# Performance work log

Measured on AMD Instinct MI355X. Metric: run time of the kernel, lower is better.

Reference implementation:

```python
import jax, jax.numpy as jnp
import numpy as np

MAX_LEN, BATCH, EMB = 512, 32, 41
HID, UNITS = 800, 20
BOND_LENS = jnp.array([1.329, 1.459, 1.525], jnp.float32)
BOND_ANGLES = jnp.array([2.034, 2.119, 1.937], jnp.float32)
INIT_ABC = jnp.array([[0.0, 0.0, 1.0], [0.0, 1.0, 0.0], [1.0, 0.0, 0.0]], jnp.float32)


def _lstm_dir(x, w_ih, w_hh, b, reverse):
    # x: [T, B, in]; returns hidden states [T, B, H]
    T, B, _ = x.shape
    H = w_hh.shape[1]
    xs = jnp.flip(x, 0) if reverse else x
    xw = jnp.einsum('tbi,gi->tbg', xs, w_ih) + b  # precompute input projection

    def step(carry, xt):
        h, c = carry
        gates = xt + h @ w_hh.T
        i, f, g, o = jnp.split(gates, 4, axis=-1)
        c = jax.nn.sigmoid(f) * c + jax.nn.sigmoid(i) * jnp.tanh(g)
        h = jax.nn.sigmoid(o) * jnp.tanh(c)
        return (h, c), h

    init = (jnp.zeros((B, H), x.dtype), jnp.zeros((B, H), x.dtype))
    _, hs = jax.lax.scan(step, init, xw)
    return jnp.flip(hs, 0) if reverse else hs


def _bilstm_layer(x, w_ih, w_hh, b):
    # w_ih: [2, 4H, in]; w_hh: [2, 4H, H]; b: [2, 4H]
    fwd = _lstm_dir(x, w_ih[0], w_hh[0], b[0], False)
    bwd = _lstm_dir(x, w_ih[1], w_hh[1], b[1], True)
    return jnp.concatenate([fwd, bwd], axis=-1)


def _geometric_unit(coords3, triplet):
    # coords3: [3, B, 3] last three atoms; triplet: [B, 3] torsion angles
    A, Bc, C = coords3[0], coords3[1], coords3[2]
    new = []
    for i in range(3):
        Tang, R, P = BOND_ANGLES[i], BOND_LENS[i], triplet[:, i]
        D2 = jnp.stack([-R * jnp.cos(Tang) * jnp.ones_like(P),
                        R * jnp.cos(P) * jnp.sin(Tang),
                        R * jnp.sin(P) * jnp.sin(Tang)], axis=1)  # [B,3]
        BC = C - Bc
        bc = BC / jnp.linalg.norm(BC, axis=1, keepdims=True)
        AB = Bc - A
        N = jnp.cross(AB, bc)
        n = N / jnp.linalg.norm(N, axis=1, keepdims=True)
        M = jnp.stack([bc, jnp.cross(n, bc), n], axis=2)  # [B,3,3]
        D = jnp.einsum('bij,bj->bi', M, D2) + C
        A, Bc, C = Bc, C, D
        new.append(D)
    return jnp.stack([A, Bc, C]), jnp.stack(new)  # carry, [3,B,3]


def setup_inputs() -> dict:
    key = jax.random.key(0)
    ks = jax.random.split(key, 10)
    k = 1.0 / np.sqrt(HID)
    u = lambda kk, shp, lim: jax.random.uniform(kk, shp, jnp.float32, -lim, lim)
    in0, in1 = EMB + 1, 2 * HID
    return {
        'sequences': jax.random.normal(ks[0], (MAX_LEN, BATCH, EMB), jnp.float32),
        'lengths': jnp.full((BATCH,), MAX_LEN, jnp.int64 if jax.config.jax_enable_x64 else jnp.int32),
        'w_ih0': u(ks[1], (2, 4 * HID, in0), k),
        'w_hh0': u(ks[2], (2, 4 * HID, HID), k),
        'b0': u(ks[3], (2, 4 * HID), k),
        'w_ih1': u(ks[4], (2, 4 * HID, in1), k),
        'w_hh1': u(ks[5], (2, 4 * HID, HID), k),
        'b1': u(ks[6], (2, 4 * HID), k),
        'lin_w': u(ks[7], (UNITS, 2 * HID), 1.0 / np.sqrt(2 * HID)),
        'lin_b': u(ks[8], (UNITS,), 1.0 / np.sqrt(2 * HID)),
        'alphabet': jax.random.uniform(ks[9], (UNITS, 3), jnp.float32, -3.14, 3.14),
    }


def reference(sequences, lengths, w_ih0, w_hh0, b0, w_ih1, w_hh1, b1, lin_w, lin_b, alphabet):
    T, B, _ = sequences.shape
    abs_pos = jnp.broadcast_to(jnp.arange(T, dtype=sequences.dtype)[:, None, None], (T, B, 1))
    x = jnp.concatenate([sequences, abs_pos], axis=2)  # [T, B, EMB+1]
    # 2-layer bidirectional LSTM (all lengths == max_len -> packing is identity)
    h = _bilstm_layer(x, w_ih0, w_hh0, b0)
    h = _bilstm_layer(h, w_ih1, w_hh1, b1)  # [T, B, 2H]
    # linear -> softmax over alphabet, trig angle decode
    soft = jax.nn.softmax(h @ lin_w.T + lin_b, axis=2)  # [T, B, UNITS]
    sine = soft @ jnp.sin(alphabet)   # [T, B, 3]
    cosine = soft @ jnp.cos(alphabet)
    out = jnp.arctan2(sine, cosine)   # torsion angle triplets
    # sequential geometric coordinate recurrence over timesteps 1..T-1
    init = jnp.broadcast_to(INIT_ABC[:, None, :], (3, B, 3))
    _, new_coords = jax.lax.scan(_geometric_unit, init, out[1:])  # [T-1, 3, B, 3]
    pred_coords = jnp.concatenate([init, new_coords.reshape(-1, B, 3)], axis=0)
    return pred_coords  # [3 + 3*(T-1), B, 3]
```

## Files before the change

### kernel.cpp

```cpp
#include <hip/hip_runtime.h>
#include <math.h>

#define T_LEN 512
#define NB    32
#define EMB_  41
#define IN0_  42
#define HID_  800
#define G4_   3200
#define IN1_  1600
#define NU    20
#define NCH   100

typedef unsigned short u16;
typedef unsigned int   u32;
typedef unsigned long long u64;
typedef __attribute__((ext_vector_type(8))) short short8;
typedef __attribute__((ext_vector_type(4))) float f32x4;

__device__ __forceinline__ float bf2f(u16 v) {
    union { u32 u; float f; } c; c.u = ((u32)v) << 16; return c.f;
}
__device__ __forceinline__ u16 f2bf(float f) {
    union { float f; u32 u; } c; c.f = f;
    u32 r = (c.u + 0x7fffu + ((c.u >> 16) & 1u)) >> 16;
    return (u16)r;
}
__device__ __forceinline__ short cvt_hl(float v, int hl) {
    u16 hi = f2bf(v);
    return hl ? (short)f2bf(v - bf2f(hi)) : (short)hi;
}
__device__ __forceinline__ f32x4 mfma16(short8 a, short8 b, f32x4 c) {
    return __builtin_amdgcn_mfma_f32_16x16x32_bf16(a, b, c, 0, 0, 0);
}
__device__ __forceinline__ u64 aload(const u64* p) {
    return __hip_atomic_load(p, __ATOMIC_RELAXED, __HIP_MEMORY_SCOPE_AGENT);
}
__device__ __forceinline__ void astore(u64* p, u64 v) {
    __hip_atomic_store(p, v, __ATOMIC_RELAXED, __HIP_MEMORY_SCOPE_AGENT);
}
__device__ __forceinline__ int afload(const int* p) {
    return __hip_atomic_load(p, __ATOMIC_RELAXED, __HIP_MEMORY_SCOPE_AGENT);
}
__device__ __forceinline__ void afstore(int* p, int v) {
    __hip_atomic_store(p, v, __ATOMIC_RELAXED, __HIP_MEMORY_SCOPE_AGENT);
}

__global__ __launch_bounds__(256, 1)
void lstm0_persist(const float* __restrict__ seq, const float* __restrict__ wih0,
                   const float* __restrict__ whh0, const float* __restrict__ bias,
                   u16* __restrict__ h0f, u16* __restrict__ hB, int* __restrict__ flags)
{
    __shared__ __align__(16) float part[2048];
    __shared__ __align__(16) u16 stageB[25600];
    __shared__ __align__(16) float w0l[32*48];
    __shared__ __align__(16) float xsl[32*48];
    __shared__ u16 hpk[NB*8];
    const int tid = threadIdx.x;
    const int d = blockIdx.x / NCH, ch = blockIdx.x % NCH;
    const int w = tid >> 6, l = tid & 63;
    const int p = w & 1, hl = w >> 1;
    int* myflags = flags + d*NCH*16;

    short8 wreg[25];
    {
        const int m = l & 15, g = p*2 + (m>>3), j = ch*8 + (m&7);
        const float* base = whh0 + ((size_t)(d*G4_ + g*HID_ + j))*HID_ + (l>>4)*8;
#pragma unroll
        for (int kc = 0; kc < 25; ++kc) {
            float4 f0 = *(const float4*)(base + kc*32);
            float4 f1 = *(const float4*)(base + kc*32 + 4);
            short8 v;
            v[0]=cvt_hl(f0.x,hl); v[1]=cvt_hl(f0.y,hl); v[2]=cvt_hl(f0.z,hl); v[3]=cvt_hl(f0.w,hl);
            v[4]=cvt_hl(f1.x,hl); v[5]=cvt_hl(f1.y,hl); v[6]=cvt_hl(f1.z,hl); v[7]=cvt_hl(f1.w,hl);
            wreg[kc] = v;
        }
    }
    for (int idx = tid; idx < 32*EMB_; idx += 256) {
        int r = idx / EMB_, k = idx % EMB_;
        int ju_ = r >> 2, g = r & 3;
        w0l[r*48 + k] = wih0[((size_t)(d*G4_ + g*HID_ + ch*8 + ju_))*IN0_ + k];
    }
    const int ju = tid >> 5, b = tid & 31;
    const int j = ch*8 + ju;
    const int nt = b >> 4, n = b & 15;
    float biasr[4], wpos[4];
#pragma unroll
    for (int g = 0; g < 4; ++g) {
        biasr[g] = bias[d*G4_ + g*HID_ + j];
        wpos[g]  = wih0[((size_t)(d*G4_ + g*HID_ + j))*IN0_ + EMB_];
    }
    float creg = 0.f;
    __syncthreads();

    for (int s = 0; s < T_LEN; ++s) {
        const int t = d ? (T_LEN-1-s) : s;
        const u64* hq64 = (const u64*)(hB + (size_t)((s&1)*2 + d)*25600);
        u64*      hnq  = (u64*)(hB + (size_t)(((s&1)^1)*2 + d)*25600);

        for (int idx = tid; idx < 32*EMB_; idx += 256)
            xsl[(idx/EMB_)*48 + idx%EMB_] = seq[(size_t)t*(NB*EMB_) + idx];

        if (s > 0 && tid < NCH)
            while (afload(myflags + tid*16) < s) __builtin_amdgcn_s_sleep(1);
        __syncthreads();

        {
            u64 tmp[25];
#pragma unroll
            for (int q = 0; q < 25; ++q) tmp[q] = aload(hq64 + tid + q*256);
#pragma unroll
            for (int q = 0; q < 25; ++q) ((u64*)stageB)[tid + q*256] = tmp[q];
        }
        __syncthreads();

        f32x4 acc0 = {0.f,0.f,0.f,0.f}, acc1 = {0.f,0.f,0.f,0.f};
#pragma unroll 5
        for (int kc = 0; kc < 25; ++kc) {
            short8 b0 = *(const short8*)(stageB + kc*1024 + l*8);
            short8 b1 = *(const short8*)(stageB + kc*1024 + 512 + l*8);
            acc0 = mfma16(wreg[kc], b0, acc0);
            acc1 = mfma16(wreg[kc], b1, acc1);
        }
        {
            const int mrow = (l>>4)*4, nn = l & 15;
#pragma unroll
            for (int r = 0; r < 4; ++r) {
                part[(((p*2+hl)*2 + 0)*16 + mrow + r)*16 + nn] = acc0[r];
                part[(((p*2+hl)*2 + 1)*16 + mrow + r)*16 + nn] = acc1[r];
            }
        }
        __syncthreads();

        float dot0 = 0.f, dot1 = 0.f, dot2 = 0.f, dot3 = 0.f;
        {
            const float* wr = &w0l[ju*4*48];
            const float* xr = &xsl[b*48];
#pragma unroll
            for (int k4 = 0; k4 < 40; k4 += 4) {
                float4 xk = *(const float4*)(xr + k4);
                float4 w0 = *(const float4*)(wr + 0*48 + k4);
                float4 w1 = *(const float4*)(wr + 1*48 + k4);
                float4 w2 = *(const float4*)(wr + 2*48 + k4);
                float4 w3 = *(const float4*)(wr + 3*48 + k4);
                dot0 += w0.x*xk.x + w0.y*xk.y + w0.z*xk.z + w0.w*xk.w;
                dot1 += w1.x*xk.x + w1.y*xk.y + w1.z*xk.z + w1.w*xk.w;
                dot2 += w2.x*xk.x + w2.y*xk.y + w2.z*xk.z + w2.w*xk.w;
                dot3 += w3.x*xk.x + w3.y*xk.y + w3.z*xk.z + w3.w*xk.w;
            }
            float xk = xr[40];
            dot0 += wr[0*48+40]*xk; dot1 += wr[1*48+40]*xk;
            dot2 += wr[2*48+40]*xk; dot3 += wr[3*48+40]*xk;
        }
        float v[4] = {dot0, dot1, dot2, dot3};
#pragma unroll
        for (int g = 0; g < 4; ++g) {
            const int pp = g >> 1, m = (g & 1)*8 + ju;
            v[g] += part[(((pp*2+0)*2 + nt)*16 + m)*16 + n]
                  + part[(((pp*2+1)*2 + nt)*16 + m)*16 + n]
                  + biasr[g] + (float)t * wpos[g];
        }
        float ig = 1.f/(1.f + expf(-v[0]));
        float fg = 1.f/(1.f + expf(-v[1]));
        float gg = tanhf(v[2]);
        float og = 1.f/(1.f + expf(-v[3]));
        creg = fg * creg + ig * gg;
        hpk[b*8 + ju] = f2bf(og * tanhf(creg));
        __syncthreads();

        u64 pk = 0; int xoff = 0;
        if (tid < 64) {
            const int bb = tid >> 1, half = tid & 1;
            const u16* hp = &hpk[bb*8 + half*4];
            pk = (u64)hp[0] | ((u64)hp[1]<<16) | ((u64)hp[2]<<32) | ((u64)hp[3]<<48);
            const int ntb = bb >> 4, llb = ((ch&3)<<4) | (bb&15);
            astore(hnq + ((ch>>2)*2 + ntb)*128 + llb*2 + half, pk);
            xoff = ((d*25 + (ch>>2))*2 + ntb)*128 + llb*2 + half;
        }
        __syncthreads();
        if (tid == 0) afstore(myflags + ch*16, s+1);
        if (tid < 64)
            ((u64*)(h0f + (size_t)t*51200))[xoff] = pk;
    }
}

__global__ __launch_bounds__(256, 1)
void lstm1_persist(const float* __restrict__ wih1, const float* __restrict__ whh1,
                   const float* __restrict__ bias, const float* __restrict__ lin_w,
                   const u16* __restrict__ h0f, u16* __restrict__ hB,
                   int* __restrict__ flags, float* __restrict__ logits)
{
    __shared__ __align__(16) u16 wihL[2*50*512];
    __shared__ __align__(16) u16 stageB[25600];
    __shared__ __align__(16) float part[2048];
    __shared__ u16 hpk[NB*8];
    const int tid = threadIdx.x;
    const int d = blockIdx.x / NCH, ch = blockIdx.x % NCH;
    const int w = tid >> 6, l = tid & 63;
    const int p = w & 1, hl = w >> 1;
    int* myflags = flags + d*NCH*16;

    short8 wreg[25];
    {
        const int m = l & 15, g = p*2 + (m>>3), j = ch*8 + (m&7);
        const float* base = whh1 + ((size_t)(d*G4_ + g*HID_ + j))*HID_ + (l>>4)*8;
#pragma unroll
        for (int kc = 0; kc < 25; ++kc) {
            float4 f0 = *(const float4*)(base + kc*32);
            float4 f1 = *(const float4*)(base + kc*32 + 4);
            short8 v;
            v[0]=cvt_hl(f0.x,hl); v[1]=cvt_hl(f0.y,hl); v[2]=cvt_hl(f0.z,hl); v[3]=cvt_hl(f0.w,hl);
            v[4]=cvt_hl(f1.x,hl); v[5]=cvt_hl(f1.y,hl); v[6]=cvt_hl(f1.z,hl); v[7]=cvt_hl(f1.w,hl);
            wreg[kc] = v;
        }
    }
    for (int o = tid; o < 6400; o += 256) {
        int pp = o / 3200, r = o % 3200, kc = r >> 6, ll = r & 63;
        int m = ll & 15, g = pp*2 + (m>>3), jj = ch*8 + (m&7);
        const float* base = wih1 + ((size_t)(d*G4_ + g*HID_ + jj))*IN1_ + kc*32 + (ll>>4)*8;
        float4 f0 = *(const float4*)base;
        float4 f1 = *(const float4*)(base + 4);
        short8 v;
        v[0]=(short)f2bf(f0.x); v[1]=(short)f2bf(f0.y); v[2]=(short)f2bf(f0.z); v[3]=(short)f2bf(f0.w);
        v[4]=(short)f2bf(f1.x); v[5]=(short)f2bf(f1.y); v[6]=(short)f2bf(f1.z); v[7]=(short)f2bf(f1.w);
        *(short8*)&wihL[o*8] = v;
    }
    const int ol = tid >> 5, ln = tid & 31;
    const int lo = ch*7 + ol;
    const bool lown = (ol < 7) && (lo < NB*NU);
    int lofs = 0;
    float wlin[25];
    if (lown) {
        const int bb = lo / NU, uu = lo % NU;
        lofs = (bb >> 4)*512 + ((((ln >> 3) << 4) | (bb & 15)))*8 + (ln & 7);
        const float* wrow = lin_w + (size_t)uu*IN1_ + d*HID_ + ln;
#pragma unroll
        for (int i = 0; i < 25; ++i) wlin[i] = wrow[i*32];
    }
    const int ju = tid >> 5, b = tid & 31;
    const int j = ch*8 + ju;
    const int nt = b >> 4, n = b & 15;
    float biasr[4];
#pragma unroll
    for (int g = 0; g < 4; ++g) biasr[g] = bias[d*G4_ + g*HID_ + j];
    float creg = 0.f;
    __syncthreads();

    for (int s = 0; s < T_LEN; ++s) {
        const int t = d ? (T_LEN-1-s) : s;
        const u64* hq64 = (const u64*)(hB + (size_t)((s&1)*2 + d)*25600);
        u64*      hnq  = (u64*)(hB + (size_t)(((s&1)^1)*2 + d)*25600);

        f32x4 acc0 = {0.f,0.f,0.f,0.f}, acc1 = {0.f,0.f,0.f,0.f};
        {
            const u16* xb = h0f + (size_t)t*51200;
#pragma unroll 5
            for (int kc = 0; kc < 25; ++kc) {
                const int idx = hl*25 + kc;
                short8 a  = *(const short8*)&wihL[(p*50 + idx)*512 + l*8];
                short8 b0 = *(const short8*)(xb + idx*1024 + l*8);
                short8 b1 = *(const short8*)(xb + idx*1024 + 512 + l*8);
                acc0 = mfma16(a, b0, acc0);
                acc1 = mfma16(a, b1, acc1);
            }
        }

        if (s > 0 && tid < NCH)
            while (afload(myflags + tid*16) < s) __builtin_amdgcn_s_sleep(1);
        __syncthreads();

        {
            u64 tmp[25];
#pragma unroll
            for (int q = 0; q < 25; ++q) tmp[q] = aload(hq64 + tid + q*256);
#pragma unroll
            for (int q = 0; q < 25; ++q) ((u64*)stageB)[tid + q*256] = tmp[q];
        }
        __syncthreads();

#pragma unroll 5
        for (int kc = 0; kc < 25; ++kc) {
            short8 b0 = *(const short8*)(stageB + kc*1024 + l*8);
            short8 b1 = *(const short8*)(stageB + kc*1024 + 512 + l*8);
            acc0 = mfma16(wreg[kc], b0, acc0);
            acc1 = mfma16(wreg[kc], b1, acc1);
        }
        {
            const int mrow = (l>>4)*4, nn = l & 15;
#pragma unroll
            for (int r = 0; r < 4; ++r) {
                part[(((p*2+hl)*2 + 0)*16 + mrow + r)*16 + nn] = acc0[r];
                part[(((p*2+hl)*2 + 1)*16 + mrow + r)*16 + nn] = acc1[r];
            }
        }
        __syncthreads();

        float v[4];
#pragma unroll
        for (int g = 0; g < 4; ++g) {
            const int pp = g >> 1, m = (g & 1)*8 + ju;
            v[g] = part[(((pp*2+0)*2 + nt)*16 + m)*16 + n]
                 + part[(((pp*2+1)*2 + nt)*16 + m)*16 + n] + biasr[g];
        }
        float ig = 1.f/(1.f + expf(-v[0]));
        float fg = 1.f/(1.f + expf(-v[1]));
        float gg = tanhf(v[2]);
        float og = 1.f/(1.f + expf(-v[3]));
        creg = fg * creg + ig * gg;
        float hn = og * tanhf(creg);
        hpk[b*8 + ju] = f2bf(hn);
        __syncthreads();

        if (tid < 64) {
            const int bb = tid >> 1, half = tid & 1;
            const u16* hp = &hpk[bb*8 + half*4];
            u64 pk = (u64)hp[0] | ((u64)hp[1]<<16) | ((u64)hp[2]<<32) | ((u64)hp[3]<<48);
            const int ntb = bb >> 4, llb = ((ch&3)<<4) | (bb&15);
            astore(hnq + ((ch>>2)*2 + ntb)*128 + llb*2 + half, pk);
        }
        __syncthreads();
        if (tid == 0) afstore(myflags + ch*16, s+1);

        if (s > 0 && lown) {
            float sum = 0.f;
#pragma unroll
            for (int i = 0; i < 25; ++i)
                sum += bf2f(stageB[i*1024 + lofs]) * wlin[i];
#pragma unroll
            for (int off2 = 16; off2; off2 >>= 1) sum += __shfl_down(sum, off2, 32);
            if (ln == 0) {
                const int tprev = d ? (T_LEN - s) : (s - 1);
                logits[((size_t)d*T_LEN + tprev)*640 + lo] = sum;
            }
        }
    }
    if (tid < NCH)
        while (afload(myflags + tid*16) < T_LEN) __builtin_amdgcn_s_sleep(1);
    __syncthreads();
    {
        const u64* hq64 = (const u64*)(hB + (size_t)((T_LEN&1)*2 + d)*25600);
        u64 tmp[25];
#pragma unroll
        for (int q = 0; q < 25; ++q) tmp[q] = aload(hq64 + tid + q*256);
#pragma unroll
        for (int q = 0; q < 25; ++q) ((u64*)stageB)[tid + q*256] = tmp[q];
    }
    __syncthreads();
    if (lown) {
        float sum = 0.f;
#pragma unroll
        for (int i = 0; i < 25; ++i)
            sum += bf2f(stageB[i*1024 + lofs]) * wlin[i];
#pragma unroll
        for (int off2 = 16; off2; off2 >>= 1) sum += __shfl_down(sum, off2, 32);
        if (ln == 0) {
            const int tprev = d ? 0 : (T_LEN - 1);
            logits[((size_t)d*T_LEN + tprev)*640 + lo] = sum;
        }
    }
}

__global__ __launch_bounds__(256)
void epilogue(const float* __restrict__ logits, const float* __restrict__ lin_b,
              const float* __restrict__ alphabet, float* __restrict__ cs)
{
    __shared__ float sa[NU*3], ca[NU*3], lb[NU];
    const int tid = threadIdx.x;
    if (tid < NU*3) { float al = alphabet[tid]; sa[tid] = sinf(al); ca[tid] = cosf(al); }
    if (tid < NU) lb[tid] = lin_b[tid];
    __syncthreads();
    const int row = blockIdx.x*256 + tid;
    if (row >= T_LEN*NB) return;
    const int t = row >> 5, b = row & 31;
    float lg[NU];
    float m = -1e30f;
#pragma unroll 4
    for (int u = 0; u < NU; ++u) {
        lg[u] = lb[u] + logits[(size_t)t*640 + b*NU + u]
                      + logits[((size_t)T_LEN + t)*640 + b*NU + u];
        m = fmaxf(m, lg[u]);
    }
    float ssum = 0.f;
#pragma unroll 4
    for (int u = 0; u < NU; ++u) { lg[u] = expf(lg[u] - m); ssum += lg[u]; }
    float inv = 1.f / ssum;
#pragma unroll
    for (int i = 0; i < 3; ++i) {
        float sv = 0.f, cv = 0.f;
#pragma unroll 4
        for (int u = 0; u < NU; ++u) {
            float sw = lg[u] * inv;
            sv += sw * sa[u*3 + i];
            cv += sw * ca[u*3 + i];
        }
        float rinv = rsqrtf(fmaxf(sv*sv + cv*cv, 1e-30f));
        *(float2*)(cs + ((size_t)row*3 + i)*2) = make_float2(cv*rinv, sv*rinv);
    }
}

__global__ __launch_bounds__(64)
void geometry(const float* __restrict__ cs, float* __restrict__ out)
{
    const int b = threadIdx.x;
    if (b >= NB) return;
    const float blen[3] = {1.329f, 1.459f, 1.525f};
    const float bang[3] = {2.034f, 2.119f, 1.937f};
    float sT[3], cT[3];
#pragma unroll
    for (int i = 0; i < 3; ++i) { sT[i] = sinf(bang[i]); cT[i] = cosf(bang[i]); }

    float Ax=0.f,Ay=0.f,Az=1.f, Bx=0.f,By=1.f,Bz=0.f, Cx=1.f,Cy=0.f,Cz=0.f;
    out[(0*NB + b)*3 + 0] = 0.f; out[(0*NB + b)*3 + 1] = 0.f; out[(0*NB + b)*3 + 2] = 1.f;
    out[(1*NB + b)*3 + 0] = 0.f; out[(1*NB + b)*3 + 1] = 1.f; out[(1*NB + b)*3 + 2] = 0.f;
    out[(2*NB + b)*3 + 0] = 1.f; out[(2*NB + b)*3 + 1] = 0.f; out[(2*NB + b)*3 + 2] = 0.f;

    for (int t = 1; t < T_LEN; ++t) {
        float2 pc[3];
#pragma unroll
        for (int i = 0; i < 3; ++i)
            pc[i] = *(const float2*)(cs + (((size_t)t*NB + b)*3 + i)*2);
#pragma unroll
        for (int i = 0; i < 3; ++i) {
            float R = blen[i];
            float d2x = -R*cT[i], d2y = R*pc[i].x*sT[i], d2z = R*pc[i].y*sT[i];
            float bcx = Cx-Bx, bcy = Cy-By, bcz = Cz-Bz;
            float inv = rsqrtf(bcx*bcx + bcy*bcy + bcz*bcz);
            bcx *= inv; bcy *= inv; bcz *= inv;
            float abx = Bx-Ax, aby = By-Ay, abz = Bz-Az;
            float nx = aby*bcz - abz*bcy;
            float ny = abz*bcx - abx*bcz;
            float nz = abx*bcy - aby*bcx;
            inv = rsqrtf(fmaxf(nx*nx + ny*ny + nz*nz, 1e-30f));
            nx *= inv; ny *= inv; nz *= inv;
            float mx = ny*bcz - nz*bcy;
            float my = nz*bcx - nx*bcz;
            float mz = nx*bcy - ny*bcx;
            float Dx = bcx*d2x + mx*d2y + nx*d2z + Cx;
            float Dy = bcy*d2x + my*d2y + ny*d2z + Cy;
            float Dz = bcz*d2x + mz*d2y + nz*d2z + Cz;
            Ax=Bx; Ay=By; Az=Bz; Bx=Cx; By=Cy; Bz=Cz; Cx=Dx; Cy=Dy; Cz=Dz;
            const int r = 3 + (t-1)*3 + i;
            out[((size_t)r*NB + b)*3 + 0] = Dx;
            out[((size_t)r*NB + b)*3 + 1] = Dy;
            out[((size_t)r*NB + b)*3 + 2] = Dz;
        }
    }
}

extern "C" void kernel_launch(void* const* d_in, const int* in_sizes, int n_in,
                              void* d_out, int out_size, void* d_ws, size_t ws_size,
                              hipStream_t stream)
{
    (void)in_sizes; (void)n_in; (void)out_size; (void)ws_size;
    const float* seq   = (const float*)d_in[0];
    const float* w_ih0 = (const float*)d_in[2];
    const float* w_hh0 = (const float*)d_in[3];
    const float* b0    = (const float*)d_in[4];
    const float* w_ih1 = (const float*)d_in[5];
    const float* w_hh1 = (const float*)d_in[6];
    const float* b1    = (const float*)d_in[7];
    const float* lin_w = (const float*)d_in[8];
    const float* lin_b = (const float*)d_in[9];
    const float* alpha = (const float*)d_in[10];

    char* ws = (char*)d_ws;
    size_t off = 0;
    u16* h0f   = (u16*)(ws + off); off += 52428800ull;
    u16* hB    = (u16*)(ws + off); off += 204800ull;
    int* flagsL0 = (int*)(ws + off); off += 12800ull;
    int* flagsL1 = (int*)(ws + off); off += 12800ull;
    float* logits = (float*)(ws + off); off += 2621440ull;
    float* cs = (float*)(ws + off); off += 393216ull;

    hipMemsetAsync(hB, 0, 204800 + 12800 + 12800, stream);

    lstm0_persist<<<dim3(2*NCH), dim3(256), 0, stream>>>(seq, w_ih0, w_hh0, b0, h0f, hB, flagsL0);

    hipMemsetAsync(hB, 0, 204800, stream);
    lstm1_persist<<<dim3(2*NCH), dim3(256), 0, stream>>>(w_ih1, w_hh1, b1, lin_w, h0f, hB,
                                                         flagsL1, logits);

    epilogue<<<dim3(64), dim3(256), 0, stream>>>(logits, lin_b, alpha, cs);
    geometry<<<dim3(1), dim3(64), 0, stream>>>(cs, (float*)d_out);
}
```

Before: 9.470 ms.

## Read recurrent state from full history buffers and pack progress flags densely

Each layer's persistent kernel drops the double-buffered hB exchange buffer. It now reads the previous step's hidden state straight from the per-timestep output history (h0f, or a new h1f for layer 1) using plain loads instead of atomic loads. Step 0 zero-fills the staging buffer. Progress flags are packed contiguously instead of padded to 64 bytes, which removes the separate state stores and a memset but may add false sharing on the flag line. Plain loads of data written by other blocks rely on the flag acquire ordering and cache coherence at agent scope, which the relaxed atomics may not guarantee.

```diff
diff --git a/kernel.cpp b/kernel.cpp
--- a/kernel.cpp
+++ b/kernel.cpp
@@ -32,9 +32,6 @@
 __device__ __forceinline__ f32x4 mfma16(short8 a, short8 b, f32x4 c) {
     return __builtin_amdgcn_mfma_f32_16x16x32_bf16(a, b, c, 0, 0, 0);
 }
-__device__ __forceinline__ u64 aload(const u64* p) {
-    return __hip_atomic_load(p, __ATOMIC_RELAXED, __HIP_MEMORY_SCOPE_AGENT);
-}
 __device__ __forceinline__ void astore(u64* p, u64 v) {
     __hip_atomic_store(p, v, __ATOMIC_RELAXED, __HIP_MEMORY_SCOPE_AGENT);
 }
@@ -44,11 +41,12 @@
 __device__ __forceinline__ void afstore(int* p, int v) {
     __hip_atomic_store(p, v, __ATOMIC_RELAXED, __HIP_MEMORY_SCOPE_AGENT);
 }
+
 
 __global__ __launch_bounds__(256, 1)
 void lstm0_persist(const float* __restrict__ seq, const float* __restrict__ wih0,
                    const float* __restrict__ whh0, const float* __restrict__ bias,
-                   u16* __restrict__ h0f, u16* __restrict__ hB, int* __restrict__ flags)
+                   u16* __restrict__ h0f, int* __restrict__ flags)
 {
     __shared__ __align__(16) float part[2048];
     __shared__ __align__(16) u16 stageB[25600];
@@ -59,7 +57,7 @@
     const int d = blockIdx.x / NCH, ch = blockIdx.x % NCH;
     const int w = tid >> 6, l = tid & 63;
     const int p = w & 1, hl = w >> 1;
-    int* myflags = flags + d*NCH*16;
+    int* myflags = flags + d*128;
 
     short8 wreg[25];
     {
@@ -94,20 +92,23 @@
 
     for (int s = 0; s < T_LEN; ++s) {
         const int t = d ? (T_LEN-1-s) : s;
-        const u64* hq64 = (const u64*)(hB + (size_t)((s&1)*2 + d)*25600);
-        u64*      hnq  = (u64*)(hB + (size_t)(((s&1)^1)*2 + d)*25600);
 
         for (int idx = tid; idx < 32*EMB_; idx += 256)
             xsl[(idx/EMB_)*48 + idx%EMB_] = seq[(size_t)t*(NB*EMB_) + idx];
 
         if (s > 0 && tid < NCH)
-            while (afload(myflags + tid*16) < s) __builtin_amdgcn_s_sleep(1);
-        __syncthreads();
-
-        {
+            while (afload(myflags + tid) < s) __builtin_amdgcn_s_sleep(1);
+        __syncthreads();
+
+        if (s == 0) {
+#pragma unroll
+            for (int q = 0; q < 25; ++q) ((u64*)stageB)[tid + q*256] = 0ull;
+        } else {
+            const int tprev = d ? (T_LEN - s) : (s - 1);
+            const u64* src = (const u64*)(h0f + (size_t)tprev*51200) + d*6400;
             u64 tmp[25];
 #pragma unroll
-            for (int q = 0; q < 25; ++q) tmp[q] = aload(hq64 + tid + q*256);
+            for (int q = 0; q < 25; ++q) tmp[q] = src[tid + q*256];
 #pragma unroll
             for (int q = 0; q < 25; ++q) ((u64*)stageB)[tid + q*256] = tmp[q];
         }
@@ -167,26 +168,23 @@
         hpk[b*8 + ju] = f2bf(og * tanhf(creg));
         __syncthreads();
 
-        u64 pk = 0; int xoff = 0;
         if (tid < 64) {
             const int bb = tid >> 1, half = tid & 1;
             const u16* hp = &hpk[bb*8 + half*4];
-            pk = (u64)hp[0] | ((u64)hp[1]<<16) | ((u64)hp[2]<<32) | ((u64)hp[3]<<48);
+            u64 pk = (u64)hp[0] | ((u64)hp[1]<<16) | ((u64)hp[2]<<32) | ((u64)hp[3]<<48);
             const int ntb = bb >> 4, llb = ((ch&3)<<4) | (bb&15);
-            astore(hnq + ((ch>>2)*2 + ntb)*128 + llb*2 + half, pk);
-            xoff = ((d*25 + (ch>>2))*2 + ntb)*128 + llb*2 + half;
-        }
-        __syncthreads();
-        if (tid == 0) afstore(myflags + ch*16, s+1);
-        if (tid < 64)
-            ((u64*)(h0f + (size_t)t*51200))[xoff] = pk;
+            const int xoff = ((d*25 + (ch>>2))*2 + ntb)*128 + llb*2 + half;
+            astore((u64*)(h0f + (size_t)t*51200) + xoff, pk);
+        }
+        __syncthreads();
+        if (tid == 0) afstore(myflags + ch, s+1);
     }
 }
 
 __global__ __launch_bounds__(256, 1)
 void lstm1_persist(const float* __restrict__ wih1, const float* __restrict__ whh1,
                    const float* __restrict__ bias, const float* __restrict__ lin_w,
-                   const u16* __restrict__ h0f, u16* __restrict__ hB,
+                   const u16* __restrict__ h0f, u16* __restrict__ h1f,
                    int* __restrict__ flags, float* __restrict__ logits)
 {
     __shared__ __align__(16) u16 wihL[2*50*512];
@@ -197,7 +195,7 @@
     const int d = blockIdx.x / NCH, ch = blockIdx.x % NCH;
     const int w = tid >> 6, l = tid & 63;
     const int p = w & 1, hl = w >> 1;
-    int* myflags = flags + d*NCH*16;
+    int* myflags = flags + d*128;
 
     short8 wreg[25];
     {
@@ -247,8 +245,6 @@
 
     for (int s = 0; s < T_LEN; ++s) {
         const int t = d ? (T_LEN-1-s) : s;
-        const u64* hq64 = (const u64*)(hB + (size_t)((s&1)*2 + d)*25600);
-        u64*      hnq  = (u64*)(hB + (size_t)(((s&1)^1)*2 + d)*25600);
 
         f32x4 acc0 = {0.f,0.f,0.f,0.f}, acc1 = {0.f,0.f,0.f,0.f};
         {
@@ -265,13 +261,18 @@
         }
 
         if (s > 0 && tid < NCH)
-            while (afload(myflags + tid*16) < s) __builtin_amdgcn_s_sleep(1);
-        __syncthreads();
-
-        {
+            while (afload(myflags + tid) < s) __builtin_amdgcn_s_sleep(1);
+        __syncthreads();
+
+        if (s == 0) {
+#pragma unroll
+            for (int q = 0; q < 25; ++q) ((u64*)stageB)[tid + q*256] = 0ull;
+        } else {
+            const int tprev = d ? (T_LEN - s) : (s - 1);
+            const u64* src = (const u64*)(h1f + (size_t)tprev*51200) + d*6400;
             u64 tmp[25];
 #pragma unroll
-            for (int q = 0; q < 25; ++q) tmp[q] = aload(hq64 + tid + q*256);
+            for (int q = 0; q < 25; ++q) tmp[q] = src[tid + q*256];
 #pragma unroll
             for (int q = 0; q < 25; ++q) ((u64*)stageB)[tid + q*256] = tmp[q];
         }
@@ -315,10 +316,11 @@
             const u16* hp = &hpk[bb*8 + half*4];
             u64 pk = (u64)hp[0] | ((u64)hp[1]<<16) | ((u64)hp[2]<<32) | ((u64)hp[3]<<48);
             const int ntb = bb >> 4, llb = ((ch&3)<<4) | (bb&15);
-            astore(hnq + ((ch>>2)*2 + ntb)*128 + llb*2 + half, pk);
-        }
-        __syncthreads();
-        if (tid == 0) afstore(myflags + ch*16, s+1);
+            const int xoff = ((d*25 + (ch>>2))*2 + ntb)*128 + llb*2 + half;
+            astore((u64*)(h1f + (size_t)t*51200) + xoff, pk);
+        }
+        __syncthreads();
+        if (tid == 0) afstore(myflags + ch, s+1);
 
         if (s > 0 && lown) {
             float sum = 0.f;
@@ -334,13 +336,14 @@
         }
     }
     if (tid < NCH)
-        while (afload(myflags + tid*16) < T_LEN) __builtin_amdgcn_s_sleep(1);
+        while (afload(myflags + tid) < T_LEN) __builtin_amdgcn_s_sleep(1);
     __syncthreads();
     {
-        const u64* hq64 = (const u64*)(hB + (size_t)((T_LEN&1)*2 + d)*25600);
+        const int tlast = d ? 0 : (T_LEN - 1);
+        const u64* src = (const u64*)(h1f + (size_t)tlast*51200) + d*6400;
         u64 tmp[25];
 #pragma unroll
-        for (int q = 0; q < 25; ++q) tmp[q] = aload(hq64 + tid + q*256);
+        for (int q = 0; q < 25; ++q) tmp[q] = src[tid + q*256];
 #pragma unroll
         for (int q = 0; q < 25; ++q) ((u64*)stageB)[tid + q*256] = tmp[q];
     }
@@ -465,18 +468,17 @@
     char* ws = (char*)d_ws;
     size_t off = 0;
     u16* h0f   = (u16*)(ws + off); off += 52428800ull;
-    u16* hB    = (u16*)(ws + off); off += 204800ull;
-    int* flagsL0 = (int*)(ws + off); off += 12800ull;
-    int* flagsL1 = (int*)(ws + off); off += 12800ull;
+    u16* h1f   = (u16*)(ws + off); off += 52428800ull;
+    int* flagsL0 = (int*)(ws + off); off += 1024ull;
+    int* flagsL1 = (int*)(ws + off); off += 1024ull;
     float* logits = (float*)(ws + off); off += 2621440ull;
     float* cs = (float*)(ws + off); off += 393216ull;
 
-    hipMemsetAsync(hB, 0, 204800 + 12800 + 12800, stream);
-
-    lstm0_persist<<<dim3(2*NCH), dim3(256), 0, stream>>>(seq, w_ih0, w_hh0, b0, h0f, hB, flagsL0);
-
-    hipMemsetAsync(hB, 0, 204800, stream);
-    lstm1_persist<<<dim3(2*NCH), dim3(256), 0, stream>>>(w_ih1, w_hh1, b1, lin_w, h0f, hB,
+    hipMemsetAsync(flagsL0, 0, 2048, stream);
+
+    lstm0_persist<<<dim3(2*NCH), dim3(256), 0, stream>>>(seq, w_ih0, w_hh0, b0, h0f, flagsL0);
+
+    lstm1_persist<<<dim3(2*NCH), dim3(256), 0, stream>>>(w_ih1, w_hh1, b1, lin_w, h0f, h1f,
                                                          flagsL1, logits);
 
     epilogue<<<dim3(64), dim3(256), 0, stream>>>(logits, lin_b, alpha, cs);
```

After: 9.387 ms. No clear change (-0.9%).
